# Optimization experiments

Hardware: AMD Instinct MI355X
Metric: run time of the kernel (lower is better)

The kernel has to match this reference:

```python
import jax, jax.numpy as jnp
import numpy as np

B, H, N, D = 4, 8, 4096, 64
M = 266  # nb_features = int(D * ln(D))
CHUNK = 128
KERNEL_EPS = 1e-4


def _gaussian_orthogonal_random_matrix(nb_rows, nb_cols, rng):
    # scaling == 0: rows are orthogonal blocks rescaled by norms of iid gaussian rows
    blocks = []
    n_full = nb_rows // nb_cols
    for _ in range(n_full):
        q, _ = np.linalg.qr(rng.standard_normal((nb_cols, nb_cols)))
        blocks.append(q.T)
    rem = nb_rows - n_full * nb_cols
    if rem > 0:
        q, _ = np.linalg.qr(rng.standard_normal((nb_cols, nb_cols)))
        blocks.append(q.T[:rem])
    final = np.concatenate(blocks, axis=0)
    multiplier = np.linalg.norm(rng.standard_normal((nb_rows, nb_cols)), axis=1)
    return (multiplier[:, None] * final).astype(np.float32)


def setup_inputs() -> dict:
    key = jax.random.key(0)
    kq, kk, kv = jax.random.split(key, 3)
    rng = np.random.default_rng(0)
    return {
        "q": jax.random.normal(kq, (B, H, N, D), dtype=jnp.float32),
        "k": jax.random.normal(kk, (B, H, N, D), dtype=jnp.float32),
        "v": jax.random.normal(kv, (B, H, N, D), dtype=jnp.float32),
        "projection_matrix": jnp.asarray(
            _gaussian_orthogonal_random_matrix(M, D, rng)),
    }


def _softmax_kernel(data, projection_matrix, is_query):
    # data: [b,h,n,d], projection: [m,d]
    d = data.shape[-1]
    data_normalizer = d ** (-0.25)
    ratio = projection_matrix.shape[0] ** (-0.5)
    data_dash = jnp.einsum('bhnd,md->bhnm', data_normalizer * data,
                           projection_matrix)
    diag_data = jnp.sum(data ** 2, axis=-1) * 0.5 * data_normalizer ** 2  # [b,h,n]
    if is_query:
        stab = jnp.max(data_dash, axis=-1, keepdims=True)
    else:
        stab = jnp.max(data_dash)  # global max, as in torch reference
    return ratio * (jnp.exp(data_dash - diag_data[..., None] - stab) + KERNEL_EPS)


def _causal_linear_attention(qp, kp, v, chunk=CHUNK):
    # qp,kp: [b,h,n,m]; v: [b,h,n,e]; chunked causal cumulative-sum scan
    b, h, n, m = qp.shape
    e = v.shape[-1]
    nc = n // chunk
    qc = qp.reshape(b, h, nc, chunk, m).transpose(2, 0, 1, 3, 4)
    kc = kp.reshape(b, h, nc, chunk, m).transpose(2, 0, 1, 3, 4)
    vc = v.reshape(b, h, nc, chunk, e).transpose(2, 0, 1, 3, 4)

    def step(carry, inp):
        k_sum, ctx_sum = carry  # [b,h,m], [b,h,m,e]
        qch, kch, vch = inp     # [b,h,c,m], [b,h,c,m], [b,h,c,e]
        k_cs = k_sum[:, :, None, :] + jnp.cumsum(kch, axis=2)  # [b,h,c,m]
        D_inv = 1.0 / jnp.einsum('bhcm,bhcm->bhc', qch, k_cs)
        ctx = ctx_sum[:, :, None] + jnp.cumsum(
            jnp.einsum('bhcm,bhce->bhcme', kch, vch), axis=2)  # [b,h,c,m,e]
        out = jnp.einsum('bhcme,bhcm,bhc->bhce', ctx, qch, D_inv)
        return (k_cs[:, :, -1], ctx[:, :, -1]), out

    init = (jnp.zeros((b, h, m), qp.dtype), jnp.zeros((b, h, m, e), qp.dtype))
    _, outs = jax.lax.scan(step, init, (qc, kc, vc))
    return outs.transpose(1, 2, 0, 3, 4).reshape(b, h, n, e)


def reference(q, k, v, projection_matrix):
    qp = _softmax_kernel(q, projection_matrix, is_query=True)
    kp = _softmax_kernel(k, projection_matrix, is_query=False)
    return _causal_linear_attention(qp, kp, v)
```

## Files before the change

### kernel.cpp

```cpp
#include <hip/hip_runtime.h>

#define BB 4
#define HH 8
#define NSEQ 4096
#define DD 64
#define MM 266
#define CCH 128
#define NCH 32
#define NBH (BB*HH)
#define NROWS (NBH*NSEQ)

#define NORMALIZER 0.35355339059327373f
#define DIAGF 0.0625f
#define RATIO 0.0613140017f
#define KEPS 1e-4f
#define SBIAS 4.0f

typedef unsigned short ushort_t;
typedef unsigned int uint_t;

typedef __attribute__((ext_vector_type(8))) short bf16x8;
typedef __attribute__((ext_vector_type(4))) float f32x4;

__device__ __forceinline__ f32x4 mfma16(bf16x8 a, bf16x8 b, f32x4 c){
  return __builtin_amdgcn_mfma_f32_16x16x32_bf16(a, b, c, 0, 0, 0);
}

__device__ __forceinline__ ushort_t f2bf(float x){
  union { float f; uint_t u; } v; v.f = x;
  uint_t r = (v.u + 0x7FFFu + ((v.u >> 16) & 1u)) >> 16;
  return (ushort_t)r;
}
__device__ __forceinline__ float bf2f(ushort_t h){
  union { uint_t u; float f; } v; v.u = ((uint_t)h) << 16;
  return v.f;
}
__device__ __forceinline__ void unpack2(uint_t w, float& lo, float& hi){
  union { uint_t u; float f; } a, b;
  a.u = w << 16; b.u = w & 0xFFFF0000u;
  lo = a.f; hi = b.f;
}

__device__ __forceinline__ bf16x8 frag_ld(const ushort_t* tile, int stride, int s0, int koff){
  const int l = threadIdx.x & 63;
  return *(const bf16x8*)(tile + (s0 + (l&15))*stride + koff + ((l>>4)<<3));
}


__global__ __launch_bounds__(256) void k_dashq(const float* __restrict__ x,
                                               const float* __restrict__ proj,
                                               ushort_t* __restrict__ qp){
  __shared__ __align__(16) ushort_t pjs[272*72];
  __shared__ __align__(16) ushort_t qs[128*72];
  __shared__ float diags[128];
  const int t = threadIdx.x;

  #pragma unroll
  for (int h=0; h<2; ++h){
    float2 pv[17];
    #pragma unroll
    for (int i=0;i<17;++i){
      int idx = t + (h*17+i)*256;
      int m = idx>>5, dp = (idx&31)*2;
      float2 p2 = {0.f,0.f};
      if (m < MM) p2 = *(const float2*)(proj + (size_t)m*DD + dp);
      pv[i] = p2;
    }
    #pragma unroll
    for (int i=0;i<17;++i){
      int idx = t + (h*17+i)*256;
      int m = idx>>5, dp = (idx&31)*2;
      *(uint_t*)(pjs + m*72 + dp) = (uint_t)f2bf(pv[i].x) | ((uint_t)f2bf(pv[i].y)<<16);
    }
  }
  {
    const int row = t>>1, half = t&1;
    const float2* xr = (const float2*)(x + ((size_t)blockIdx.x*128 + row)*DD + half*32);
    float ss = 0.f;
    #pragma unroll
    for (int i=0;i<16;++i){
      float2 a = xr[i];
      ss += a.x*a.x + a.y*a.y;
      uint_t w = (uint_t)f2bf(a.x*NORMALIZER) | ((uint_t)f2bf(a.y*NORMALIZER)<<16);
      *(uint_t*)(qs + row*72 + half*32 + i*2) = w;
    }
    ss += __shfl_xor(ss, 1);
    if (half==0) diags[row] = ss*DIAGF;
  }
  __syncthreads();

  const int l = t&63, wv = t>>6;
  const int wr0 = wv*32;
  float dv[2][4];
  #pragma unroll
  for (int rt=0;rt<2;++rt)
    #pragma unroll
    for (int r=0;r<4;++r) dv[rt][r] = diags[wr0 + rt*16 + ((l>>4)<<2) + r];

  float rmax[2][4];
  #pragma unroll
  for (int rt=0;rt<2;++rt){ rmax[rt][0]=-3e38f; rmax[rt][1]=-3e38f; rmax[rt][2]=-3e38f; rmax[rt][3]=-3e38f; }
  for (int mt=0; mt<17; ++mt){
    bf16x8 b0 = frag_ld(pjs, 72, mt*16, 0);
    bf16x8 b1 = frag_ld(pjs, 72, mt*16, 32);
    const bool valid = (mt*16 + (l&15)) < MM;
    #pragma unroll
    for (int rt=0;rt<2;++rt){
      bf16x8 a0 = frag_ld(qs, 72, wr0+rt*16, 0);
      bf16x8 a1 = frag_ld(qs, 72, wr0+rt*16, 32);
      f32x4 acc = {0.f,0.f,0.f,0.f};
      acc = mfma16(a0, b0, acc);
      acc = mfma16(a1, b1, acc);
      #pragma unroll
      for (int r=0;r<4;++r){
        float sp = acc[r] - dv[rt][r] + SBIAS;
        if (valid) rmax[rt][r] = fmaxf(rmax[rt][r], sp);
      }
    }
  }
  float sub[2][4];
  #pragma unroll
  for (int rt=0;rt<2;++rt){
    #pragma unroll
    for (int r=0;r<4;++r){
      float m = rmax[rt][r];
      m = fmaxf(m, __shfl_xor(m,1)); m = fmaxf(m, __shfl_xor(m,2));
      m = fmaxf(m, __shfl_xor(m,4)); m = fmaxf(m, __shfl_xor(m,8));
      sub[rt][r] = m + dv[rt][r];
    }
  }

  const size_t growb = (size_t)blockIdx.x*128;
  for (int mt=0; mt<17; ++mt){
    bf16x8 b0 = frag_ld(pjs, 72, mt*16, 0);
    bf16x8 b1 = frag_ld(pjs, 72, mt*16, 32);
    const int m = mt*16 + (l&15);
    #pragma unroll
    for (int rt=0;rt<2;++rt){
      bf16x8 a0 = frag_ld(qs, 72, wr0+rt*16, 0);
      bf16x8 a1 = frag_ld(qs, 72, wr0+rt*16, 32);
      f32x4 acc = {0.f,0.f,0.f,0.f};
      acc = mfma16(a0, b0, acc);
      acc = mfma16(a1, b1, acc);
      if (m < MM){
        #pragma unroll
        for (int r=0;r<4;++r){
          float sp = acc[r] - dv[rt][r] + SBIAS;
          float e = RATIO*(__expf(bf2f(f2bf(sp)) - sub[rt][r]) + KEPS);
          qp[(growb + wr0 + rt*16 + ((l>>4)<<2) + r)*MM + m] = f2bf(e);
        }
      }
    }
  }
}


__global__ __launch_bounds__(256) void k_dashk(const float* __restrict__ x,
                                               const float* __restrict__ proj,
                                               ushort_t* __restrict__ sbuf,
                                               float* __restrict__ rowsub){
  __shared__ __align__(16) ushort_t pjs[272*72];
  __shared__ __align__(16) ushort_t qs[128*72];
  __shared__ float diags[128];
  const int t = threadIdx.x;

  #pragma unroll
  for (int h=0; h<2; ++h){
    float2 pv[17];
    #pragma unroll
    for (int i=0;i<17;++i){
      int idx = t + (h*17+i)*256;
      int m = idx>>5, dp = (idx&31)*2;
      float2 p2 = {0.f,0.f};
      if (m < MM) p2 = *(const float2*)(proj + (size_t)m*DD + dp);
      pv[i] = p2;
    }
    #pragma unroll
    for (int i=0;i<17;++i){
      int idx = t + (h*17+i)*256;
      int m = idx>>5, dp = (idx&31)*2;
      *(uint_t*)(pjs + m*72 + dp) = (uint_t)f2bf(pv[i].x) | ((uint_t)f2bf(pv[i].y)<<16);
    }
  }
  {
    const int row = t>>1, half = t&1;
    const float2* xr = (const float2*)(x + ((size_t)blockIdx.x*128 + row)*DD + half*32);
    float ss = 0.f;
    #pragma unroll
    for (int i=0;i<16;++i){
      float2 a = xr[i];
      ss += a.x*a.x + a.y*a.y;
      uint_t w = (uint_t)f2bf(a.x*NORMALIZER) | ((uint_t)f2bf(a.y*NORMALIZER)<<16);
      *(uint_t*)(qs + row*72 + half*32 + i*2) = w;
    }
    ss += __shfl_xor(ss, 1);
    if (half==0) diags[row] = ss*DIAGF;
  }
  __syncthreads();

  const int l = t&63, wv = t>>6;
  const int wr0 = wv*32;
  float dv[2][4];
  #pragma unroll
  for (int rt=0;rt<2;++rt)
    #pragma unroll
    for (int r=0;r<4;++r) dv[rt][r] = diags[wr0 + rt*16 + ((l>>4)<<2) + r];

  float rmax[2][4];
  #pragma unroll
  for (int rt=0;rt<2;++rt){ rmax[rt][0]=-3e38f; rmax[rt][1]=-3e38f; rmax[rt][2]=-3e38f; rmax[rt][3]=-3e38f; }

  const size_t growb = (size_t)blockIdx.x*128;
  for (int mt=0; mt<17; ++mt){
    bf16x8 b0 = frag_ld(pjs, 72, mt*16, 0);
    bf16x8 b1 = frag_ld(pjs, 72, mt*16, 32);
    const int m = mt*16 + (l&15);
    const bool valid = (m < MM);
    #pragma unroll
    for (int rt=0;rt<2;++rt){
      bf16x8 a0 = frag_ld(qs, 72, wr0+rt*16, 0);
      bf16x8 a1 = frag_ld(qs, 72, wr0+rt*16, 32);
      f32x4 acc = {0.f,0.f,0.f,0.f};
      acc = mfma16(a0, b0, acc);
      acc = mfma16(a1, b1, acc);
      #pragma unroll
      for (int r=0;r<4;++r){
        float sp = acc[r] - dv[rt][r] + SBIAS;
        if (valid){
          rmax[rt][r] = fmaxf(rmax[rt][r], sp);
          sbuf[(growb + wr0 + rt*16 + ((l>>4)<<2) + r)*MM + m] = f2bf(sp);
        }
      }
    }
  }
  #pragma unroll
  for (int rt=0;rt<2;++rt){
    #pragma unroll
    for (int r=0;r<4;++r){
      float m = rmax[rt][r];
      m = fmaxf(m, __shfl_xor(m,1)); m = fmaxf(m, __shfl_xor(m,2));
      m = fmaxf(m, __shfl_xor(m,4)); m = fmaxf(m, __shfl_xor(m,8));
      if ((l&15)==0)
        rowsub[growb + wr0 + rt*16 + ((l>>4)<<2) + r] = m + dv[rt][r];
    }
  }
}


__global__ __launch_bounds__(256) void k_gmax1(const float* __restrict__ rowsub,
                                               float* __restrict__ part){
  __shared__ float s[4];
  int t = threadIdx.x;
  float m = rowsub[(size_t)blockIdx.x*256 + t];
  #pragma unroll
  for (int off=32; off>0; off>>=1) m = fmaxf(m, __shfl_xor(m, off));
  if ((t&63)==0) s[t>>6] = m;
  __syncthreads();
  if (t==0) part[blockIdx.x] = fmaxf(fmaxf(s[0],s[1]), fmaxf(s[2],s[3]));
}

__global__ __launch_bounds__(256) void k_gmax2(const float* __restrict__ part,
                                               float* __restrict__ gmax){
  __shared__ float s[4];
  int t = threadIdx.x;
  float m = fmaxf(part[t], part[t+256]);
  #pragma unroll
  for (int off=32; off>0; off>>=1) m = fmaxf(m, __shfl_xor(m, off));
  if ((t&63)==0) s[t>>6] = m;
  __syncthreads();
  if (t==0) gmax[0] = fmaxf(fmaxf(s[0],s[1]), fmaxf(s[2],s[3]));
}


__global__ __launch_bounds__(256) void k_chunksum3(const ushort_t* __restrict__ kd,
                                                   const float* __restrict__ v,
                                                   const float* __restrict__ gmaxp,
                                                   ushort_t* __restrict__ ctx,
                                                   float* __restrict__ z){
  __shared__ __align__(16) ushort_t kpT[272*34];
  __shared__ __align__(16) ushort_t vT[64*136];
  const int blk = blockIdx.x, bh = blk>>5, ch = blk&31;
  const int t = threadIdx.x, l = t&63, wv = t>>6;
  const int row0 = ch*CCH;
  const ushort_t* kg = kd + (size_t)(bh*NSEQ + row0)*MM;
  const float*    vg = v  + (size_t)(bh*NSEQ + row0)*DD;
  const float g = gmaxp[0];

  {
    const int e = t&63, r0i = t>>6;
    float rv[32];
    #pragma unroll
    for (int i=0;i<32;++i) rv[i] = vg[(size_t)(r0i + 4*i)*DD + e];
    #pragma unroll
    for (int i=0;i<32;++i) vT[e*136 + r0i + 4*i] = f2bf(rv[i]);
  }

  f32x4 acc[17];
  #pragma unroll
  for (int i=0;i<17;++i) acc[i] = (f32x4){0.f,0.f,0.f,0.f};
  float zacc = 0.f, zacc2 = 0.f;
  const bool hasz2 = (256 + t) < MM;

  for (int ks=0; ks<4; ++ks){
    __syncthreads();
    {
      ushort_t rv[40];
      #pragma unroll
      for (int rr=0; rr<8; ++rr){
        const ushort_t* src = kg + (size_t)(ks*32 + wv*8 + rr)*MM;
        #pragma unroll
        for (int j=0;j<5;++j){
          int m = l + j*64;
          rv[rr*5+j] = (m < MM) ? src[m] : (ushort_t)0;
        }
      }
      #pragma unroll
      for (int rr=0; rr<8; ++rr){
        #pragma unroll
        for (int j=0;j<5;++j){
          int m = l + j*64;
          if (m < 272){
            ushort_t o = 0;
            if (m < MM) o = f2bf(RATIO*(__expf(bf2f(rv[rr*5+j]) - g) + KEPS));
            kpT[m*34 + wv*8 + rr] = o;
          }
        }
      }
    }
    __syncthreads();
    {
      float s1 = 0.f, s2 = 0.f;
      #pragma unroll
      for (int r=0;r<32;++r){
        s1 += bf2f(kpT[t*34 + r]);
        if (t < 16) s2 += bf2f(kpT[(256+t)*34 + r]);
      }
      zacc += s1; zacc2 += s2;
    }
    bf16x8 bv = frag_ld(vT, 136, wv*16, ks*32);
    #pragma unroll
    for (int mt=0; mt<17; ++mt){
      bf16x8 a = frag_ld(kpT, 34, mt*16, 0);
      acc[mt] = mfma16(a, bv, acc[mt]);
    }
  }

  ushort_t* cg = ctx + (size_t)blk*MM*DD;
  const int e = wv*16 + (l&15);
  #pragma unroll
  for (int mt=0; mt<17; ++mt){
    #pragma unroll
    for (int r=0;r<4;++r){
      int m = mt*16 + ((l>>4)<<2) + r;
      if (m < MM) cg[(size_t)m*DD + e] = f2bf(acc[mt][r]);
    }
  }
  float* zgo = z + (size_t)blk*MM;
  zgo[t] = zacc;
  if (hasz2) zgo[256+t] = zacc2;
}


__global__ __launch_bounds__(256) void k_prefix_ctx2(ushort_t* __restrict__ ctx){
  int blk = blockIdx.x; int bh = blk/67, mg = blk%67;
  int t = threadIdx.x; int mo = t>>6, e = t&63;
  int m = mg*4 + mo;
  if (m >= MM) return;
  size_t base = (size_t)bh*NCH*MM*DD + (size_t)m*DD + e;
  float vals[32];
  #pragma unroll
  for (int c=0;c<NCH;++c) vals[c] = bf2f(ctx[base + (size_t)c*MM*DD]);
  float run = 0.f;
  #pragma unroll
  for (int c=0;c<NCH;++c){
    float cur = vals[c];
    ctx[base + (size_t)c*MM*DD] = f2bf(run);
    run += cur;
  }
}

__global__ __launch_bounds__(256) void k_prefix_z2(float* __restrict__ z){
  int bh = blockIdx.x, t = threadIdx.x;
  size_t base = (size_t)bh*NCH*MM;
  {
    float va[32];
    #pragma unroll
    for (int c=0;c<NCH;++c) va[c] = z[base + (size_t)c*MM + t];
    float run = 0.f;
    #pragma unroll
    for (int c=0;c<NCH;++c){ float cur = va[c]; z[base + (size_t)c*MM + t] = run; run += cur; }
  }
  if (256 + t < MM){
    float vb[32];
    #pragma unroll
    for (int c=0;c<NCH;++c) vb[c] = z[base + (size_t)c*MM + 256 + t];
    float run = 0.f;
    #pragma unroll
    for (int c=0;c<NCH;++c){ float cur = vb[c]; z[base + (size_t)c*MM + 256 + t] = run; run += cur; }
  }
}


__global__ __launch_bounds__(256) void k_output7(const ushort_t* __restrict__ qp,
                                                 const ushort_t* __restrict__ kd,
                                                 const float* __restrict__ v,
                                                 const ushort_t* __restrict__ ctx,
                                                 const float* __restrict__ z,
                                                 const float* __restrict__ gmaxp,
                                                 float* __restrict__ out){
  __shared__ __align__(16) char lds[54272];
  ushort_t* qs   = (ushort_t*)lds;
  ushort_t* kss  = (ushort_t*)(lds + 18432);
  ushort_t* Ps   = (ushort_t*)lds;
  ushort_t* ctxT = (ushort_t*)(lds + 36864);
  ushort_t* vT   = (ushort_t*)(lds + 36864);

  const int blk = blockIdx.x, bh = blk>>5, ch = blk&31;
  const int t = threadIdx.x, l = t&63, wv = t>>6;
  const int row0 = ch*CCH;
  const int wr0 = wv*32;
  const float g = gmaxp[0];

  const ushort_t* qg = qp + (size_t)(bh*NSEQ + row0)*MM;
  const ushort_t* kg = kd + (size_t)(bh*NSEQ + row0)*MM;
  const float*    vg = v  + (size_t)(bh*NSEQ + row0)*DD;
  const ushort_t* ctxg = ctx + (size_t)blk*MM*DD;
  const float*    zg = z  + (size_t)blk*MM;

  const int mcol  = (t&31)<<1;
  const int qrow0 = t>>5;
  const int ce    = t&63;
  const int cm0   = t>>6;
  uint_t rq[16], rk[16];
  ushort_t rc[16];
  float rz;

#define LOADREGS(MT) do{ \
    const int m0_ = (MT)*64; \
    const bool vq_ = (m0_ + mcol) < MM; \
    _Pragma("unroll") \
    for (int i=0;i<16;++i){ \
      int row_ = qrow0 + 8*i; \
      rq[i] = vq_ ? *(const uint_t*)(qg + (size_t)row_*MM + m0_ + mcol) : 0u; \
      rk[i] = vq_ ? *(const uint_t*)(kg + (size_t)row_*MM + m0_ + mcol) : 0u; \
    } \
    _Pragma("unroll") \
    for (int i=0;i<16;++i){ \
      int mm_ = cm0 + 4*i; \
      rc[i] = (m0_ + mm_ < MM) ? ctxg[(size_t)(m0_ + mm_)*DD + ce] : (ushort_t)0; \
    } \
    rz = (m0_ + (t&63) < MM) ? zg[m0_ + (t&63)] : 0.f; \
  }while(0)

#define WRITELDS(MT) do{ \
    const int m0_ = (MT)*64; \
    const bool vq_ = (m0_ + mcol) < MM; \
    _Pragma("unroll") \
    for (int i=0;i<16;++i){ \
      int row_ = qrow0 + 8*i; \
      *(uint_t*)(qs + row_*72 + mcol) = rq[i]; \
      uint_t ko_ = 0u; \
      if (vq_){ \
        float a_, b_; unpack2(rk[i], a_, b_); \
        a_ = RATIO*(__expf(a_ - g) + KEPS); \
        b_ = RATIO*(__expf(b_ - g) + KEPS); \
        ko_ = (uint_t)f2bf(a_) | ((uint_t)f2bf(b_)<<16); \
      } \
      *(uint_t*)(kss + row_*72 + mcol) = ko_; \
    } \
    _Pragma("unroll") \
    for (int i=0;i<16;++i) ctxT[ce*72 + cm0 + 4*i] = rc[i]; \
    if (t < 64) ctxT[64*72 + t] = f2bf(rz); \
  }while(0)

  for (int idx=t; idx<15*72; idx+=256) ctxT[65*72 + idx] = 0;

  f32x4 acc[2][8];
  f32x4 oacc[2][5];
  #pragma unroll
  for (int rt=0;rt<2;++rt){
    #pragma unroll
    for (int ct=0;ct<8;++ct) acc[rt][ct] = (f32x4){0.f,0.f,0.f,0.f};
    #pragma unroll
    for (int et=0;et<5;++et) oacc[rt][et] = (f32x4){0.f,0.f,0.f,0.f};
  }

  LOADREGS(0);
  for (int mt=0; mt<5; ++mt){
    __syncthreads();
    WRITELDS(mt);
    __syncthreads();
    if (mt < 4) LOADREGS(mt+1);

    bf16x8 aq[2][2];
    #pragma unroll
    for (int rt=0;rt<2;++rt){
      aq[rt][0] = frag_ld(qs, 72, wr0+rt*16, 0);
      aq[rt][1] = frag_ld(qs, 72, wr0+rt*16, 32);
    }
    #pragma unroll
    for (int ct=0;ct<8;++ct){
      bf16x8 b0 = frag_ld(kss, 72, ct*16, 0);
      bf16x8 b1 = frag_ld(kss, 72, ct*16, 32);
      #pragma unroll
      for (int rt=0;rt<2;++rt){
        acc[rt][ct] = mfma16(aq[rt][0], b0, acc[rt][ct]);
        acc[rt][ct] = mfma16(aq[rt][1], b1, acc[rt][ct]);
      }
    }
    #pragma unroll
    for (int et=0;et<5;++et){
      bf16x8 b0 = frag_ld(ctxT, 72, et*16, 0);
      bf16x8 b1 = frag_ld(ctxT, 72, et*16, 32);
      #pragma unroll
      for (int rt=0;rt<2;++rt){
        oacc[rt][et] = mfma16(aq[rt][0], b0, oacc[rt][et]);
        oacc[rt][et] = mfma16(aq[rt][1], b1, oacc[rt][et]);
      }
    }
  }
  __syncthreads();

  float rv[32];
  {
    const int e = t&63, r0i = t>>6;
    #pragma unroll
    for (int i=0;i<32;++i) rv[i] = vg[(size_t)(r0i + 4*i)*DD + e];
  }

  float ds[2][4];
  #pragma unroll
  for (int rt=0;rt<2;++rt){ ds[rt][0]=0.f; ds[rt][1]=0.f; ds[rt][2]=0.f; ds[rt][3]=0.f; }
  #pragma unroll
  for (int rt=0;rt<2;++rt){
    #pragma unroll
    for (int ct=0;ct<8;++ct){
      #pragma unroll
      for (int r=0;r<4;++r){
        int i = wr0 + rt*16 + ((l>>4)<<2) + r;
        int j = ct*16 + (l&15);
        float m = (j <= i) ? acc[rt][ct][r] : 0.f;
        acc[rt][ct][r] = m;
        ds[rt][r] += m;
      }
    }
  }
  #pragma unroll
  for (int rt=0;rt<2;++rt){
    #pragma unroll
    for (int ct=0;ct<8;++ct){
      #pragma unroll
      for (int r=0;r<4;++r){
        int i = wr0 + rt*16 + ((l>>4)<<2) + r;
        Ps[i*136 + ct*16 + (l&15)] = f2bf(acc[rt][ct][r]);
      }
    }
  }
  float dtot[2][4];
  #pragma unroll
  for (int rt=0;rt<2;++rt){
    #pragma unroll
    for (int r=0;r<4;++r){
      float d = ds[rt][r];
      d += __shfl_xor(d,1); d += __shfl_xor(d,2); d += __shfl_xor(d,4); d += __shfl_xor(d,8);
      dtot[rt][r] = d + __shfl(oacc[rt][4][r], l & 48);
    }
  }
  {
    const int e = t&63, r0i = t>>6;
    #pragma unroll
    for (int i=0;i<32;++i) vT[e*136 + r0i + 4*i] = f2bf(rv[i]);
  }
  __syncthreads();

  #pragma unroll
  for (int kt=0;kt<4;++kt){
    bf16x8 ap[2];
    #pragma unroll
    for (int rt=0;rt<2;++rt) ap[rt] = frag_ld(Ps, 136, wr0+rt*16, kt*32);
    #pragma unroll
    for (int et=0;et<4;++et){
      bf16x8 bv = frag_ld(vT, 136, et*16, kt*32);
      #pragma unroll
      for (int rt=0;rt<2;++rt) oacc[rt][et] = mfma16(ap[rt], bv, oacc[rt][et]);
    }
  }

  float* og = out + (size_t)(bh*NSEQ + row0)*DD;
  #pragma unroll
  for (int rt=0;rt<2;++rt){
    #pragma unroll
    for (int r=0;r<4;++r){
      int i = wr0 + rt*16 + ((l>>4)<<2) + r;
      float dinv = 1.0f / dtot[rt][r];
      #pragma unroll
      for (int et=0;et<4;++et)
        og[(size_t)i*DD + et*16 + (l&15)] = oacc[rt][et][r] * dinv;
    }
  }
#undef LOADREGS
#undef WRITELDS
}


extern "C" void kernel_launch(void* const* d_in, const int* in_sizes, int n_in,
                              void* d_out, int out_size, void* d_ws, size_t ws_size,
                              hipStream_t stream) {
  const float* q    = (const float*)d_in[0];
  const float* k    = (const float*)d_in[1];
  const float* v    = (const float*)d_in[2];
  const float* proj = (const float*)d_in[3];
  float* out = (float*)d_out;
  char* ws = (char*)d_ws;

  const size_t QP_OFF   = 0;
  const size_t KD_OFF   = 69730304ull;
  const size_t CTX_OFF  = 139460608ull;
  const size_t Z_OFF    = 174325760ull;
  const size_t RSUB_OFF = 175415296ull;
  const size_t PART_OFF = 175939584ull;
  const size_t GMAX_OFF = 175941632ull;
  if (ws_size < 175942000ull) return;

  ushort_t* qp   = (ushort_t*)(ws + QP_OFF);
  ushort_t* kd   = (ushort_t*)(ws + KD_OFF);
  ushort_t* ctx  = (ushort_t*)(ws + CTX_OFF);
  float* z       = (float*)(ws + Z_OFF);
  float* rowsub  = (float*)(ws + RSUB_OFF);
  float* part    = (float*)(ws + PART_OFF);
  float* gmax    = (float*)(ws + GMAX_OFF);

  k_dashq <<<NROWS/128, 256, 0, stream>>>(q, proj, qp);
  k_dashk <<<NROWS/128, 256, 0, stream>>>(k, proj, kd, rowsub);
  k_gmax1 <<<512, 256, 0, stream>>>(rowsub, part);
  k_gmax2 <<<1, 256, 0, stream>>>(part, gmax);
  k_chunksum3 <<<NBH*NCH, 256, 0, stream>>>(kd, v, gmax, ctx, z);
  k_prefix_ctx2<<<NBH*67, 256, 0, stream>>>(ctx);
  k_prefix_z2 <<<NBH, 256, 0, stream>>>(z);
  k_output7   <<<NBH*NCH, 256, 0, stream>>>(qp, kd, v, ctx, z, gmax, out);
}
```

Before: 247.5 us.

## Recompute query features inside output kernel instead of materializing qp

The query dash kernel now writes only the per-row max and diagonal terms. The output kernel recomputes the query feature map per 64-column slice, using MFMA against a bf16 projection copied into LDS, and applies the exp there. This avoids writing and re-reading the large bf16 qp buffer (about 70 MB). In exchange it adds a small projection-conversion kernel, redundant MFMA and exp work in the output kernel, an extra barrier per slice, and more LDS, which may lower occupancy.

```diff
diff --git a/kernel.cpp b/kernel.cpp
--- a/kernel.cpp
+++ b/kernel.cpp
@@ -47,9 +47,25 @@
 }
 
 
-__global__ __launch_bounds__(256) void k_dashq(const float* __restrict__ x,
-                                               const float* __restrict__ proj,
-                                               ushort_t* __restrict__ qp){
+__global__ __launch_bounds__(256) void k_projbf(const float* __restrict__ proj,
+                                                ushort_t* __restrict__ projbf){
+  int idx = blockIdx.x*256 + threadIdx.x;
+  if (idx >= 320*36) return;
+  int row = idx/36, cu = idx - row*36;
+  int dp = cu*2;
+  uint_t w = 0;
+  if (row < MM && dp < DD){
+    float2 p2 = *(const float2*)(proj + (size_t)row*DD + dp);
+    w = (uint_t)f2bf(p2.x) | ((uint_t)f2bf(p2.y)<<16);
+  }
+  ((uint_t*)projbf)[idx] = w;
+}
+
+
+__global__ __launch_bounds__(256) void k_dashqmax(const float* __restrict__ x,
+                                                  const float* __restrict__ proj,
+                                                  float* __restrict__ rowsub,
+                                                  float* __restrict__ diagq){
   __shared__ __align__(16) ushort_t pjs[272*72];
   __shared__ __align__(16) ushort_t qs[128*72];
   __shared__ float diags[128];
@@ -73,9 +89,10 @@
       *(uint_t*)(pjs + m*72 + dp) = (uint_t)f2bf(pv[i].x) | ((uint_t)f2bf(pv[i].y)<<16);
     }
   }
+  const size_t growb = (size_t)blockIdx.x*128;
   {
     const int row = t>>1, half = t&1;
-    const float2* xr = (const float2*)(x + ((size_t)blockIdx.x*128 + row)*DD + half*32);
+    const float2* xr = (const float2*)(x + (growb + row)*DD + half*32);
     float ss = 0.f;
     #pragma unroll
     for (int i=0;i<16;++i){
@@ -85,7 +102,7 @@
       *(uint_t*)(qs + row*72 + half*32 + i*2) = w;
     }
     ss += __shfl_xor(ss, 1);
-    if (half==0) diags[row] = ss*DIAGF;
+    if (half==0){ diags[row] = ss*DIAGF; diagq[growb + row] = ss*DIAGF; }
   }
   __syncthreads();
 
@@ -100,6 +117,7 @@
   float rmax[2][4];
   #pragma unroll
   for (int rt=0;rt<2;++rt){ rmax[rt][0]=-3e38f; rmax[rt][1]=-3e38f; rmax[rt][2]=-3e38f; rmax[rt][3]=-3e38f; }
+
   for (int mt=0; mt<17; ++mt){
     bf16x8 b0 = frag_ld(pjs, 72, mt*16, 0);
     bf16x8 b1 = frag_ld(pjs, 72, mt*16, 32);
@@ -118,7 +136,6 @@
       }
     }
   }
-  float sub[2][4];
   #pragma unroll
   for (int rt=0;rt<2;++rt){
     #pragma unroll
@@ -126,30 +143,8 @@
       float m = rmax[rt][r];
       m = fmaxf(m, __shfl_xor(m,1)); m = fmaxf(m, __shfl_xor(m,2));
       m = fmaxf(m, __shfl_xor(m,4)); m = fmaxf(m, __shfl_xor(m,8));
-      sub[rt][r] = m + dv[rt][r];
-    }
-  }
-
-  const size_t growb = (size_t)blockIdx.x*128;
-  for (int mt=0; mt<17; ++mt){
-    bf16x8 b0 = frag_ld(pjs, 72, mt*16, 0);
-    bf16x8 b1 = frag_ld(pjs, 72, mt*16, 32);
-    const int m = mt*16 + (l&15);
-    #pragma unroll
-    for (int rt=0;rt<2;++rt){
-      bf16x8 a0 = frag_ld(qs, 72, wr0+rt*16, 0);
-      bf16x8 a1 = frag_ld(qs, 72, wr0+rt*16, 32);
-      f32x4 acc = {0.f,0.f,0.f,0.f};
-      acc = mfma16(a0, b0, acc);
-      acc = mfma16(a1, b1, acc);
-      if (m < MM){
-        #pragma unroll
-        for (int r=0;r<4;++r){
-          float sp = acc[r] - dv[rt][r] + SBIAS;
-          float e = RATIO*(__expf(bf2f(f2bf(sp)) - sub[rt][r]) + KEPS);
-          qp[(growb + wr0 + rt*16 + ((l>>4)<<2) + r)*MM + m] = f2bf(e);
-        }
-      }
+      if ((l&15)==0)
+        rowsub[growb + wr0 + rt*16 + ((l>>4)<<2) + r] = m + dv[rt][r];
     }
   }
 }
@@ -401,18 +396,22 @@
 }
 
 
-__global__ __launch_bounds__(256) void k_output7(const ushort_t* __restrict__ qp,
+__global__ __launch_bounds__(256) void k_output8(const float* __restrict__ q,
                                                  const ushort_t* __restrict__ kd,
                                                  const float* __restrict__ v,
                                                  const ushort_t* __restrict__ ctx,
                                                  const float* __restrict__ z,
                                                  const float* __restrict__ gmaxp,
+                                                 const ushort_t* __restrict__ projbf,
+                                                 const float* __restrict__ rowsubq,
+                                                 const float* __restrict__ diagq,
                                                  float* __restrict__ out){
-  __shared__ __align__(16) char lds[54272];
+  __shared__ __align__(16) char lds[57600];
   ushort_t* qs   = (ushort_t*)lds;
   ushort_t* kss  = (ushort_t*)(lds + 18432);
   ushort_t* Ps   = (ushort_t*)lds;
-  ushort_t* ctxT = (ushort_t*)(lds + 36864);
+  ushort_t* pj   = (ushort_t*)(lds + 36864);
+  ushort_t* ctxT = (ushort_t*)(lds + 46080);
   ushort_t* vT   = (ushort_t*)(lds + 36864);
 
   const int blk = blockIdx.x, bh = blk>>5, ch = blk&31;
@@ -421,17 +420,48 @@
   const int wr0 = wv*32;
   const float g = gmaxp[0];
 
-  const ushort_t* qg = qp + (size_t)(bh*NSEQ + row0)*MM;
   const ushort_t* kg = kd + (size_t)(bh*NSEQ + row0)*MM;
   const float*    vg = v  + (size_t)(bh*NSEQ + row0)*DD;
   const ushort_t* ctxg = ctx + (size_t)blk*MM*DD;
   const float*    zg = z  + (size_t)blk*MM;
 
+  bf16x8 qx[2][2];
+  {
+    const float* qgf = q + (size_t)(bh*NSEQ + row0)*DD;
+    #pragma unroll
+    for (int rt=0;rt<2;++rt){
+      const int row = wr0 + rt*16 + (l&15);
+      #pragma unroll
+      for (int kh=0;kh<2;++kh){
+        const float4* p4 = (const float4*)(qgf + (size_t)row*DD + kh*32 + ((l>>4)<<3));
+        float4 a = p4[0], b = p4[1];
+        union { ushort_t s[8]; bf16x8 v8; } u;
+        u.s[0]=f2bf(a.x*NORMALIZER); u.s[1]=f2bf(a.y*NORMALIZER);
+        u.s[2]=f2bf(a.z*NORMALIZER); u.s[3]=f2bf(a.w*NORMALIZER);
+        u.s[4]=f2bf(b.x*NORMALIZER); u.s[5]=f2bf(b.y*NORMALIZER);
+        u.s[6]=f2bf(b.z*NORMALIZER); u.s[7]=f2bf(b.w*NORMALIZER);
+        qx[rt][kh] = u.v8;
+      }
+    }
+  }
+  float subv[2][4], dvv[2][4];
+  {
+    const size_t rb = (size_t)bh*NSEQ + row0 + wr0;
+    #pragma unroll
+    for (int rt=0;rt<2;++rt){
+      size_t idx = rb + rt*16 + ((l>>4)<<2);
+      float4 s4 = *(const float4*)(rowsubq + idx);
+      float4 d4 = *(const float4*)(diagq + idx);
+      subv[rt][0]=s4.x; subv[rt][1]=s4.y; subv[rt][2]=s4.z; subv[rt][3]=s4.w;
+      dvv[rt][0]=d4.x; dvv[rt][1]=d4.y; dvv[rt][2]=d4.z; dvv[rt][3]=d4.w;
+    }
+  }
+
   const int mcol  = (t&31)<<1;
   const int qrow0 = t>>5;
   const int ce    = t&63;
   const int cm0   = t>>6;
-  uint_t rq[16], rk[16];
+  uint_t rk[16];
   ushort_t rc[16];
   float rz;
 
@@ -441,7 +471,6 @@
     _Pragma("unroll") \
     for (int i=0;i<16;++i){ \
       int row_ = qrow0 + 8*i; \
-      rq[i] = vq_ ? *(const uint_t*)(qg + (size_t)row_*MM + m0_ + mcol) : 0u; \
       rk[i] = vq_ ? *(const uint_t*)(kg + (size_t)row_*MM + m0_ + mcol) : 0u; \
     } \
     _Pragma("unroll") \
@@ -458,7 +487,6 @@
     _Pragma("unroll") \
     for (int i=0;i<16;++i){ \
       int row_ = qrow0 + 8*i; \
-      *(uint_t*)(qs + row_*72 + mcol) = rq[i]; \
       uint_t ko_ = 0u; \
       if (vq_){ \
         float a_, b_; unpack2(rk[i], a_, b_); \
@@ -471,6 +499,13 @@
     _Pragma("unroll") \
     for (int i=0;i<16;++i) ctxT[ce*72 + cm0 + 4*i] = rc[i]; \
     if (t < 64) ctxT[64*72 + t] = f2bf(rz); \
+    {  \
+      const uint_t* pbu = (const uint_t*)projbf; \
+      const int rl_ = t>>2, c0u_ = (t&3)*9; \
+      _Pragma("unroll") \
+      for (int j=0;j<9;++j) \
+        *(uint_t*)(pj + rl_*72 + (c0u_+j)*2) = pbu[(size_t)(m0_+rl_)*36 + c0u_ + j]; \
+    } \
   }while(0)
 
   for (int idx=t; idx<15*72; idx+=256) ctxT[65*72 + idx] = 0;
@@ -489,6 +524,26 @@
   for (int mt=0; mt<5; ++mt){
     __syncthreads();
     WRITELDS(mt);
+    __syncthreads();
+
+    #pragma unroll
+    for (int sub=0; sub<4; ++sub){
+      bf16x8 b0 = frag_ld(pj, 72, sub*16, 0);
+      bf16x8 b1 = frag_ld(pj, 72, sub*16, 32);
+      #pragma unroll
+      for (int rt=0;rt<2;++rt){
+        f32x4 da = {0.f,0.f,0.f,0.f};
+        da = mfma16(qx[rt][0], b0, da);
+        da = mfma16(qx[rt][1], b1, da);
+        #pragma unroll
+        for (int r=0;r<4;++r){
+          int row = wr0 + rt*16 + ((l>>4)<<2) + r;
+          float sp = da[r] - dvv[rt][r] + SBIAS;
+          float e = RATIO*(__expf(bf2f(f2bf(sp)) - subv[rt][r]) + KEPS);
+          qs[row*72 + sub*16 + (l&15)] = f2bf(e);
+        }
+      }
+    }
     __syncthreads();
     if (mt < 4) LOADREGS(mt+1);
 
@@ -613,29 +668,35 @@
   float* out = (float*)d_out;
   char* ws = (char*)d_ws;
 
-  const size_t QP_OFF   = 0;
-  const size_t KD_OFF   = 69730304ull;
-  const size_t CTX_OFF  = 139460608ull;
-  const size_t Z_OFF    = 174325760ull;
-  const size_t RSUB_OFF = 175415296ull;
-  const size_t PART_OFF = 175939584ull;
-  const size_t GMAX_OFF = 175941632ull;
-  if (ws_size < 175942000ull) return;
-
-  ushort_t* qp   = (ushort_t*)(ws + QP_OFF);
-  ushort_t* kd   = (ushort_t*)(ws + KD_OFF);
-  ushort_t* ctx  = (ushort_t*)(ws + CTX_OFF);
-  float* z       = (float*)(ws + Z_OFF);
-  float* rowsub  = (float*)(ws + RSUB_OFF);
-  float* part    = (float*)(ws + PART_OFF);
-  float* gmax    = (float*)(ws + GMAX_OFF);
-
-  k_dashq <<<NROWS/128, 256, 0, stream>>>(q, proj, qp);
-  k_dashk <<<NROWS/128, 256, 0, stream>>>(k, proj, kd, rowsub);
-  k_gmax1 <<<512, 256, 0, stream>>>(rowsub, part);
-  k_gmax2 <<<1, 256, 0, stream>>>(part, gmax);
-  k_chunksum3 <<<NBH*NCH, 256, 0, stream>>>(kd, v, gmax, ctx, z);
+  const size_t KD_OFF    = 0;
+  const size_t CTX_OFF   = 69730304ull;
+  const size_t Z_OFF     = 104595456ull;
+  const size_t RSUBK_OFF = 105684992ull;
+  const size_t RSUBQ_OFF = 106209280ull;
+  const size_t DIAGQ_OFF = 106733568ull;
+  const size_t PART_OFF  = 107257856ull;
+  const size_t GMAX_OFF  = 107259904ull;
+  const size_t PROJBF_OFF= 107260160ull;
+  if (ws_size < 107306300ull) return;
+
+  ushort_t* kd     = (ushort_t*)(ws + KD_OFF);
+  ushort_t* ctx    = (ushort_t*)(ws + CTX_OFF);
+  float* z         = (float*)(ws + Z_OFF);
+  float* rowsubk   = (float*)(ws + RSUBK_OFF);
+  float* rowsubq   = (float*)(ws + RSUBQ_OFF);
+  float* diagq     = (float*)(ws + DIAGQ_OFF);
+  float* part      = (float*)(ws + PART_OFF);
+  float* gmax      = (float*)(ws + GMAX_OFF);
+  ushort_t* projbf = (ushort_t*)(ws + PROJBF_OFF);
+
+  k_projbf   <<<45, 256, 0, stream>>>(proj, projbf);
+  k_dashqmax <<<NROWS/128, 256, 0, stream>>>(q, proj, rowsubq, diagq);
+  k_dashk    <<<NROWS/128, 256, 0, stream>>>(k, proj, kd, rowsubk);
+  k_gmax1    <<<512, 256, 0, stream>>>(rowsubk, part);
+  k_gmax2    <<<1, 256, 0, stream>>>(part, gmax);
+  k_chunksum3<<<NBH*NCH, 256, 0, stream>>>(kd, v, gmax, ctx, z);
   k_prefix_ctx2<<<NBH*67, 256, 0, stream>>>(ctx);
-  k_prefix_z2 <<<NBH, 256, 0, stream>>>(z);
-  k_output7   <<<NBH*NCH, 256, 0, stream>>>(qp, kd, v, ctx, z, gmax, out);
-}
+  k_prefix_z2<<<NBH, 256, 0, stream>>>(z);
+  k_output8  <<<NBH*NCH, 256, 0, stream>>>(q, kd, v, ctx, z, gmax, projbf,
+                                           rowsubq, diagq, out);
+}
```

Result: slower. 259.0 us (+4.6%).

## Use 512 threads per block in output kernel, computing the z term with scalar dot products

Applied to the files above, without the earlier changes.

The output kernel now runs 8 waves per block, each owning 16 rows instead of 32, which halves per-thread register arrays and accumulators. The q·z normaliser term is no longer folded in as an extra MFMA column tile of ctx. Instead z is staged in LDS and each lane does a scalar dot product, followed by a cross-lane reduction. This aims to raise occupancy and latency hiding and to drop the wasted fifth MFMA tile, at the cost of more scalar FMAs and LDS reads per thread.

```diff
diff --git a/kernel.cpp b/kernel.cpp
--- a/kernel.cpp
+++ b/kernel.cpp
@@ -401,7 +401,7 @@
 }
 
 
-__global__ __launch_bounds__(256) void k_output7(const ushort_t* __restrict__ qp,
+__global__ __launch_bounds__(512) void k_output9(const ushort_t* __restrict__ qp,
                                                  const ushort_t* __restrict__ kd,
                                                  const float* __restrict__ v,
                                                  const ushort_t* __restrict__ ctx,
@@ -413,12 +413,13 @@
   ushort_t* kss  = (ushort_t*)(lds + 18432);
   ushort_t* Ps   = (ushort_t*)lds;
   ushort_t* ctxT = (ushort_t*)(lds + 36864);
+  float*    zs   = (float*)(lds + 46080);
   ushort_t* vT   = (ushort_t*)(lds + 36864);
 
   const int blk = blockIdx.x, bh = blk>>5, ch = blk&31;
   const int t = threadIdx.x, l = t&63, wv = t>>6;
   const int row0 = ch*CCH;
-  const int wr0 = wv*32;
+  const int wr0 = wv*16;
   const float g = gmaxp[0];
 
   const ushort_t* qg = qp + (size_t)(bh*NSEQ + row0)*MM;
@@ -427,37 +428,37 @@
   const ushort_t* ctxg = ctx + (size_t)blk*MM*DD;
   const float*    zg = z  + (size_t)blk*MM;
 
+  for (int i=t;i<320;i+=512) zs[i] = (i<MM) ? zg[i] : 0.f;
+
   const int mcol  = (t&31)<<1;
   const int qrow0 = t>>5;
   const int ce    = t&63;
   const int cm0   = t>>6;
-  uint_t rq[16], rk[16];
-  ushort_t rc[16];
-  float rz;
+  uint_t rq[8], rk[8];
+  ushort_t rc[8];
 
 #define LOADREGS(MT) do{ \
     const int m0_ = (MT)*64; \
     const bool vq_ = (m0_ + mcol) < MM; \
     _Pragma("unroll") \
-    for (int i=0;i<16;++i){ \
-      int row_ = qrow0 + 8*i; \
+    for (int i=0;i<8;++i){ \
+      int row_ = qrow0 + 16*i; \
       rq[i] = vq_ ? *(const uint_t*)(qg + (size_t)row_*MM + m0_ + mcol) : 0u; \
       rk[i] = vq_ ? *(const uint_t*)(kg + (size_t)row_*MM + m0_ + mcol) : 0u; \
     } \
     _Pragma("unroll") \
-    for (int i=0;i<16;++i){ \
-      int mm_ = cm0 + 4*i; \
+    for (int i=0;i<8;++i){ \
+      int mm_ = cm0 + 8*i; \
       rc[i] = (m0_ + mm_ < MM) ? ctxg[(size_t)(m0_ + mm_)*DD + ce] : (ushort_t)0; \
     } \
-    rz = (m0_ + (t&63) < MM) ? zg[m0_ + (t&63)] : 0.f; \
   }while(0)
 
 #define WRITELDS(MT) do{ \
     const int m0_ = (MT)*64; \
     const bool vq_ = (m0_ + mcol) < MM; \
     _Pragma("unroll") \
-    for (int i=0;i<16;++i){ \
-      int row_ = qrow0 + 8*i; \
+    for (int i=0;i<8;++i){ \
+      int row_ = qrow0 + 16*i; \
       *(uint_t*)(qs + row_*72 + mcol) = rq[i]; \
       uint_t ko_ = 0u; \
       if (vq_){ \
@@ -469,21 +470,16 @@
       *(uint_t*)(kss + row_*72 + mcol) = ko_; \
     } \
     _Pragma("unroll") \
-    for (int i=0;i<16;++i) ctxT[ce*72 + cm0 + 4*i] = rc[i]; \
-    if (t < 64) ctxT[64*72 + t] = f2bf(rz); \
+    for (int i=0;i<8;++i) ctxT[ce*72 + cm0 + 8*i] = rc[i]; \
   }while(0)
 
-  for (int idx=t; idx<15*72; idx+=256) ctxT[65*72 + idx] = 0;
-
-  f32x4 acc[2][8];
-  f32x4 oacc[2][5];
-  #pragma unroll
-  for (int rt=0;rt<2;++rt){
-    #pragma unroll
-    for (int ct=0;ct<8;++ct) acc[rt][ct] = (f32x4){0.f,0.f,0.f,0.f};
-    #pragma unroll
-    for (int et=0;et<5;++et) oacc[rt][et] = (f32x4){0.f,0.f,0.f,0.f};
-  }
+  f32x4 acc[8];
+  f32x4 oacc[4];
+  #pragma unroll
+  for (int ct=0;ct<8;++ct) acc[ct] = (f32x4){0.f,0.f,0.f,0.f};
+  #pragma unroll
+  for (int et=0;et<4;++et) oacc[et] = (f32x4){0.f,0.f,0.f,0.f};
+  float dzacc = 0.f;
 
   LOADREGS(0);
   for (int mt=0; mt<5; ++mt){
@@ -492,111 +488,95 @@
     __syncthreads();
     if (mt < 4) LOADREGS(mt+1);
 
-    bf16x8 aq[2][2];
-    #pragma unroll
-    for (int rt=0;rt<2;++rt){
-      aq[rt][0] = frag_ld(qs, 72, wr0+rt*16, 0);
-      aq[rt][1] = frag_ld(qs, 72, wr0+rt*16, 32);
+    bf16x8 aq[2];
+    aq[0] = frag_ld(qs, 72, wr0, 0);
+    aq[1] = frag_ld(qs, 72, wr0, 32);
+    #pragma unroll
+    for (int kh=0;kh<2;++kh){
+      const int mb = mt*64 + kh*32 + ((l>>4)<<3);
+      #pragma unroll
+      for (int j=0;j<8;++j)
+        dzacc += bf2f((ushort_t)aq[kh][j]) * zs[mb + j];
     }
     #pragma unroll
     for (int ct=0;ct<8;++ct){
       bf16x8 b0 = frag_ld(kss, 72, ct*16, 0);
       bf16x8 b1 = frag_ld(kss, 72, ct*16, 32);
-      #pragma unroll
-      for (int rt=0;rt<2;++rt){
-        acc[rt][ct] = mfma16(aq[rt][0], b0, acc[rt][ct]);
-        acc[rt][ct] = mfma16(aq[rt][1], b1, acc[rt][ct]);
-      }
-    }
-    #pragma unroll
-    for (int et=0;et<5;++et){
+      acc[ct] = mfma16(aq[0], b0, acc[ct]);
+      acc[ct] = mfma16(aq[1], b1, acc[ct]);
+    }
+    #pragma unroll
+    for (int et=0;et<4;++et){
       bf16x8 b0 = frag_ld(ctxT, 72, et*16, 0);
       bf16x8 b1 = frag_ld(ctxT, 72, et*16, 32);
-      #pragma unroll
-      for (int rt=0;rt<2;++rt){
-        oacc[rt][et] = mfma16(aq[rt][0], b0, oacc[rt][et]);
-        oacc[rt][et] = mfma16(aq[rt][1], b1, oacc[rt][et]);
-      }
+      oacc[et] = mfma16(aq[0], b0, oacc[et]);
+      oacc[et] = mfma16(aq[1], b1, oacc[et]);
     }
   }
   __syncthreads();
 
-  float rv[32];
+  dzacc += __shfl_xor(dzacc, 16);
+  dzacc += __shfl_xor(dzacc, 32);
+
+  float rv[16];
   {
     const int e = t&63, r0i = t>>6;
     #pragma unroll
-    for (int i=0;i<32;++i) rv[i] = vg[(size_t)(r0i + 4*i)*DD + e];
-  }
-
-  float ds[2][4];
-  #pragma unroll
-  for (int rt=0;rt<2;++rt){ ds[rt][0]=0.f; ds[rt][1]=0.f; ds[rt][2]=0.f; ds[rt][3]=0.f; }
-  #pragma unroll
-  for (int rt=0;rt<2;++rt){
-    #pragma unroll
-    for (int ct=0;ct<8;++ct){
-      #pragma unroll
-      for (int r=0;r<4;++r){
-        int i = wr0 + rt*16 + ((l>>4)<<2) + r;
-        int j = ct*16 + (l&15);
-        float m = (j <= i) ? acc[rt][ct][r] : 0.f;
-        acc[rt][ct][r] = m;
-        ds[rt][r] += m;
-      }
-    }
-  }
-  #pragma unroll
-  for (int rt=0;rt<2;++rt){
-    #pragma unroll
-    for (int ct=0;ct<8;++ct){
-      #pragma unroll
-      for (int r=0;r<4;++r){
-        int i = wr0 + rt*16 + ((l>>4)<<2) + r;
-        Ps[i*136 + ct*16 + (l&15)] = f2bf(acc[rt][ct][r]);
-      }
-    }
-  }
-  float dtot[2][4];
-  #pragma unroll
-  for (int rt=0;rt<2;++rt){
+    for (int i=0;i<16;++i) rv[i] = vg[(size_t)(r0i + 8*i)*DD + e];
+  }
+
+  float ds[4] = {0.f,0.f,0.f,0.f};
+  #pragma unroll
+  for (int ct=0;ct<8;++ct){
     #pragma unroll
     for (int r=0;r<4;++r){
-      float d = ds[rt][r];
-      d += __shfl_xor(d,1); d += __shfl_xor(d,2); d += __shfl_xor(d,4); d += __shfl_xor(d,8);
-      dtot[rt][r] = d + __shfl(oacc[rt][4][r], l & 48);
-    }
+      int i = wr0 + ((l>>4)<<2) + r;
+      int j = ct*16 + (l&15);
+      float m = (j <= i) ? acc[ct][r] : 0.f;
+      acc[ct][r] = m;
+      ds[r] += m;
+    }
+  }
+  #pragma unroll
+  for (int ct=0;ct<8;++ct){
+    #pragma unroll
+    for (int r=0;r<4;++r){
+      int i = wr0 + ((l>>4)<<2) + r;
+      Ps[i*136 + ct*16 + (l&15)] = f2bf(acc[ct][r]);
+    }
+  }
+  float dtot[4];
+  #pragma unroll
+  for (int r=0;r<4;++r){
+    float d = ds[r];
+    d += __shfl_xor(d,1); d += __shfl_xor(d,2); d += __shfl_xor(d,4); d += __shfl_xor(d,8);
+    dtot[r] = d + __shfl(dzacc, ((l>>4)<<2) + r);
   }
   {
     const int e = t&63, r0i = t>>6;
     #pragma unroll
-    for (int i=0;i<32;++i) vT[e*136 + r0i + 4*i] = f2bf(rv[i]);
+    for (int i=0;i<16;++i) vT[e*136 + r0i + 8*i] = f2bf(rv[i]);
   }
   __syncthreads();
 
   #pragma unroll
   for (int kt=0;kt<4;++kt){
-    bf16x8 ap[2];
-    #pragma unroll
-    for (int rt=0;rt<2;++rt) ap[rt] = frag_ld(Ps, 136, wr0+rt*16, kt*32);
+    bf16x8 ap = frag_ld(Ps, 136, wr0, kt*32);
     #pragma unroll
     for (int et=0;et<4;++et){
       bf16x8 bv = frag_ld(vT, 136, et*16, kt*32);
-      #pragma unroll
-      for (int rt=0;rt<2;++rt) oacc[rt][et] = mfma16(ap[rt], bv, oacc[rt][et]);
+      oacc[et] = mfma16(ap, bv, oacc[et]);
     }
   }
 
   float* og = out + (size_t)(bh*NSEQ + row0)*DD;
   #pragma unroll
-  for (int rt=0;rt<2;++rt){
-    #pragma unroll
-    for (int r=0;r<4;++r){
-      int i = wr0 + rt*16 + ((l>>4)<<2) + r;
-      float dinv = 1.0f / dtot[rt][r];
-      #pragma unroll
-      for (int et=0;et<4;++et)
-        og[(size_t)i*DD + et*16 + (l&15)] = oacc[rt][et][r] * dinv;
-    }
+  for (int r=0;r<4;++r){
+    int i = wr0 + ((l>>4)<<2) + r;
+    float dinv = 1.0f / dtot[r];
+    #pragma unroll
+    for (int et=0;et<4;++et)
+      og[(size_t)i*DD + et*16 + (l&15)] = oacc[et][r] * dinv;
   }
 #undef LOADREGS
 #undef WRITELDS
@@ -637,5 +617,5 @@
   k_chunksum3 <<<NBH*NCH, 256, 0, stream>>>(kd, v, gmax, ctx, z);
   k_prefix_ctx2<<<NBH*67, 256, 0, stream>>>(ctx);
   k_prefix_z2 <<<NBH, 256, 0, stream>>>(z);
-  k_output7   <<<NBH*NCH, 256, 0, stream>>>(qp, kd, v, ctx, z, gmax, out);
-}
+  k_output9   <<<NBH*NCH, 512, 0, stream>>>(qp, kd, v, ctx, z, gmax, out);
+}
```

Result: faster. 231.1 us (-6.6%).
